# Optimization experiments

Measured on AMD Instinct MI355X. Metric: run time of the kernel, lower is better.

## Reference

```python
import jax, jax.numpy as jnp
import numpy as np

PAD_VAL = -999
N_TYPES = 8
D_IN, D_FF, D_FFC = 512, 1024, 512
B, S = 64, 512


def setup_inputs() -> dict:
    key = jax.random.key(0)
    ks = jax.random.split(key, 6)
    sc = 0.02
    return {
        "x": jax.random.normal(ks[0], (B, S, D_IN), dtype=jnp.float32),
        "sc_types": jax.random.randint(ks[1], (B, S), 0, N_TYPES, dtype=jnp.int64),
        "W_pre": jax.random.normal(ks[2], (D_IN, D_FF), dtype=jnp.float32) * sc,
        "W_types": jax.random.normal(ks[3], (N_TYPES, D_FF, D_IN), dtype=jnp.float32) * sc,
        "W_c1": jax.random.normal(ks[4], (D_IN, D_FFC), dtype=jnp.float32) * sc,
        "W_c2": jax.random.normal(ks[5], (D_FFC, 1), dtype=jnp.float32) * sc,
    }


def reference(x, sc_types, W_pre, W_types, W_c1, W_c2):
    # flatten tokens: [B*S, d_in], [B*S]
    x = x.reshape(-1, x.shape[-1])
    t = sc_types.reshape(-1)
    # (inputs contain no PAD_VAL tokens, so the pad mask is all-True and the
    # gather x[mask] is the identity; shapes stay static)
    x_ = jax.nn.relu(x @ W_pre)                       # [N, d_ff]
    # hard type routing: select per-type MLP output for each token
    x_types = jnp.zeros_like(x)
    for i in range(N_TYPES):
        yi = jax.nn.relu(x_ @ W_types[i])             # [N, d_in]
        x_types = jnp.where((t == i)[:, None], yi, x_types)
    x = x + x_types                                    # residual combine
    h = jax.nn.relu(x @ W_c1)                          # [N, d_ffc]
    return h @ W_c2                                    # [N, 1]
```

## Files before the change

kernel.cpp:

```cpp
#include <hip/hip_runtime.h>
#include <stdint.h>

#define N_TOK 32768
#define DIN   512
#define DFF   1024
#define MPAD  33792

__device__ __forceinline__ int rotk(int k, int row) {
    return (k & ~127) + (((k & 127) + ((row & 15) << 3)) & 127);
}

typedef __attribute__((ext_vector_type(8))) short bf16x8;
typedef __attribute__((ext_vector_type(4))) float f32x4;

__device__ __forceinline__ unsigned short f2bf(float f) {
    union { float f; unsigned int u; } v; v.f = f;
    unsigned int u = v.u;
    return (unsigned short)((u + 0x7FFFu + ((u >> 16) & 1u)) >> 16);
}
__device__ __forceinline__ float bf2f(unsigned int bits) {
    union { unsigned int u; float f; } v; v.u = bits << 16; return v.f;
}
__device__ __forceinline__ unsigned int pk4_fp8(float a, float b, float c, float d) {
    int v = __builtin_amdgcn_cvt_pk_fp8_f32(a, b, 0, false);
    v = __builtin_amdgcn_cvt_pk_fp8_f32(c, d, v, true);
    return (unsigned int)v;
}
__device__ __forceinline__ unsigned char f2fp8(float a) {
    return (unsigned char)(__builtin_amdgcn_cvt_pk_fp8_f32(a, a, 0, false) & 0xFF);
}

__device__ __forceinline__ void async16(const void* g, void* l) {
    __builtin_amdgcn_global_load_lds(
        (const __attribute__((address_space(1))) void*)g,
        (__attribute__((address_space(3))) void*)l, 16, 0, 0);
}

__global__ void prep_kernel(const float* __restrict__ x,
                            unsigned short* __restrict__ Xb,
                            unsigned char* __restrict__ Xb8,
                            const int* __restrict__ types,
                            int* __restrict__ blockhist,
                            const float* __restrict__ Wp,
                            const float* __restrict__ Wt,
                            const float* __restrict__ Wc,
                            unsigned char* __restrict__ Wp8,
                            unsigned char* __restrict__ Wt8,
                            unsigned short* __restrict__ WcT,
                            int* __restrict__ perm) {
    __shared__ float tile[32][33];
    __shared__ int lc[8];
    const int b = blockIdx.x, tid = threadIdx.x;
    if (b < 16384) {
        const int i = b * 1024 + tid * 4;
        float4 v = *(const float4*)(x + i);
        ushort4 o;
        o.x = f2bf(v.x); o.y = f2bf(v.y); o.z = f2bf(v.z); o.w = f2bf(v.w);
        *(ushort4*)(Xb + i) = o;
        const int row = i >> 9;
        const int k   = i & 511;
        *(unsigned int*)(Xb8 + (size_t)row * DIN + rotk(k, row)) = pk4_fp8(v.x, v.y, v.z, v.w);
        if (b < 64) {
            if (tid < 8) lc[tid] = 0;
            __syncthreads();
            atomicAdd(&lc[types[b * 512 + tid]], 1);
            atomicAdd(&lc[types[b * 512 + 256 + tid]], 1);
            __syncthreads();
            if (tid < 8) blockhist[b * 8 + tid] = lc[tid];
        }
    } else if (b < 26624) {
        const int r = b - 16384;
        const int z = r >> 10;
        const int bx = r & 31, by = (r >> 5) & 31;
        const int tx = tid & 31, ty = tid >> 5;
        const float* s; int K, N;
        if (z == 0)      { s = Wp;                          K = 512;  N = 1024; }
        else if (z <= 8) { s = Wt + (size_t)(z-1)*DIN*DFF;  K = 1024; N = 512; }
        else             { s = Wc;                          K = 512;  N = 512; }
        const int n0 = bx * 32, k0 = by * 32;
        if (n0 >= N || k0 >= K) return;
        for (int i = ty; i < 32; i += 8)
            tile[i][tx] = s[(size_t)(k0 + i) * N + n0 + tx];
        __syncthreads();
        if (z == 0) {
            for (int i = ty; i < 32; i += 8) {
                int n = n0 + i;
                Wp8[(size_t)n * K + rotk(k0 + tx, n)] = f2fp8(tile[tx][i] * 64.f);
            }
        } else if (z <= 8) {
            unsigned char* d = Wt8 + (size_t)(z-1)*DIN*DFF;
            for (int i = ty; i < 32; i += 8) {
                int n = n0 + i;
                d[(size_t)n * K + rotk(k0 + tx, n)] = f2fp8(tile[tx][i] * 64.f);
            }
        } else {
            for (int i = ty; i < 32; i += 8)
                WcT[(size_t)(n0 + i) * K + k0 + tx] = f2bf(tile[tx][i]);
        }
    } else {
        perm[(b - 26624) * 256 + tid] = -1;
    }
}

__global__ void scatter_kernel(const int* __restrict__ types,
                               const int* __restrict__ blockhist,
                               int* __restrict__ perm,
                               int* __restrict__ invperm,
                               float* __restrict__ outz,
                               int* __restrict__ po_out) {
    __shared__ int tots[8], base[8], fill[8];
    const int blk = blockIdx.x;
    const int tid = threadIdx.x;
    const int i = blk * 512 + tid;
    outz[i] = 0.f;
    int pre = 0;
    if (tid < 8) {
        int total = 0;
        for (int j = 0; j < 64; j++) {
            int v = blockhist[j * 8 + tid];
            if (j < blk) pre += v;
            total += v;
        }
        tots[tid] = total;
    }
    __syncthreads();
    if (tid < 8) {
        int off = 0, pob = 0;
        #pragma unroll
        for (int t2 = 0; t2 < 8; t2++) {
            if (t2 == tid) pob = off;
            off += ((tots[t2] + 127) >> 7) << 7;
        }
        base[tid] = pob + pre;
        fill[tid] = 0;
        if (blk == 0) {
            po_out[tid] = pob;
            if (tid == 0) po_out[8] = off;
        }
    }
    __syncthreads();
    const int t = types[i];
    const int r = atomicAdd(&fill[t], 1);
    const int p = base[t] + r;
    perm[p] = i;
    invperm[i] = p;
}

__global__ __launch_bounds__(512, 2)
void gemm1_fp8_8ph(const unsigned char* __restrict__ A,
                   const unsigned char* __restrict__ B,
                   unsigned char* __restrict__ C8,
                   const int* __restrict__ invperm) {
    __shared__ unsigned char As[2][256 * 128];
    __shared__ unsigned char Bs[2][256 * 128];
    __shared__ int ptile[256];

    const int tid  = threadIdx.x;
    const int wave = tid >> 6;
    const int lane = tid & 63;
    const int quad = lane >> 4;
    const int tl   = lane & 15;

    const int lin  = blockIdx.x;
    const int sid  = (lin & 7) * 64 + (lin >> 3);
    const int m0   = (sid >> 2) * 256;
    const int n0   = (sid & 3) * 256;

    const int wm = (wave & 1) * 128;
    const int wn = (wave >> 1) * 64;

    if (tid < 256) ptile[tid] = invperm[m0 + tid];

    f32x4 acc[8][4];
    #pragma unroll
    for (int i = 0; i < 8; i++)
        #pragma unroll
        for (int j = 0; j < 4; j++)
            acc[i][j] = (f32x4){0.f, 0.f, 0.f, 0.f};

    #pragma unroll
    for (int ci = 0; ci < 8; ++ci) {
        const int c = ci * 512 + tid;
        if (ci < 4) {
            const int row = c >> 3, j = c & 7;
            async16(A + (size_t)(m0 + row) * 512 + j * 16, &As[0][c * 16]);
        } else {
            const int c2 = c - 2048;
            const int row = c2 >> 3, j = c2 & 7;
            async16(B + (size_t)(n0 + row) * 512 + j * 16, &Bs[0][c2 * 16]);
        }
    }
    asm volatile("s_waitcnt vmcnt(0)" ::: "memory");
    __builtin_amdgcn_s_barrier();
    asm volatile("" ::: "memory");

    for (int t = 0; t < 4; ++t) {
        const unsigned char* Asl = As[t & 1];
        const unsigned char* Bsl = Bs[t & 1];
        unsigned char* Asn = As[(t + 1) & 1];
        unsigned char* Bsn = Bs[(t + 1) & 1];
        const int k0n = (t + 1) * 128;
        const bool st = (t < 3);
        #pragma unroll
        for (int ph = 0; ph < 8; ++ph) {
            const int ks = ph >> 1, mh = ph & 1;
            const int o = (ks * 32 + quad * 8 + tl * 8) & 127;
            long af[4], bfr[4];
            #pragma unroll
            for (int mt = 0; mt < 4; ++mt)
                af[mt] = *(const long*)(Asl + (wm + mh * 64 + mt * 16 + tl) * 128 + o);
            #pragma unroll
            for (int nt = 0; nt < 4; ++nt)
                bfr[nt] = *(const long*)(Bsl + (wn + nt * 16 + tl) * 128 + o);
            if (st && ph < 4) {
                #pragma unroll
                for (int u = 0; u < 2; ++u) {
                    const int cidx = ph * 2 + u;
                    const int c = cidx * 512 + tid;
                    if (cidx < 4) {
                        const int row = c >> 3, j = c & 7;
                        async16(A + (size_t)(m0 + row) * 512 + k0n + j * 16, Asn + c * 16);
                    } else {
                        const int c2 = c - 2048;
                        const int row = c2 >> 3, j = c2 & 7;
                        async16(B + (size_t)(n0 + row) * 512 + k0n + j * 16, Bsn + c2 * 16);
                    }
                }
            }
            __builtin_amdgcn_s_barrier();
            asm volatile("" ::: "memory");
            __builtin_amdgcn_s_setprio(1);
            #pragma unroll
            for (int mt = 0; mt < 4; ++mt)
                #pragma unroll
                for (int nt = 0; nt < 4; ++nt)
                    acc[mh * 4 + mt][nt] = __builtin_amdgcn_mfma_f32_16x16x32_fp8_fp8(
                        bfr[nt], af[mt], acc[mh * 4 + mt][nt], 0, 0, 0);
            __builtin_amdgcn_s_setprio(0);
            if (ph == 7) asm volatile("s_waitcnt vmcnt(0)" ::: "memory");
            __builtin_amdgcn_s_barrier();
            asm volatile("" ::: "memory");
        }
    }

    #pragma unroll
    for (int mh = 0; mh < 2; ++mh)
        #pragma unroll
        for (int mt = 0; mt < 4; ++mt) {
            const int p = ptile[wm + mh * 64 + mt * 16 + tl];
            const size_t rowbase = (size_t)p * DFF;
            const int prot = (p & 15) << 3;
            #pragma unroll
            for (int nt = 0; nt < 4; ++nt) {
                const int off = wn + nt * 16 + quad * 4;
                unsigned int pk = pk4_fp8(fmaxf(acc[mh * 4 + mt][nt][0], 0.f) * 0.125f,
                                          fmaxf(acc[mh * 4 + mt][nt][1], 0.f) * 0.125f,
                                          fmaxf(acc[mh * 4 + mt][nt][2], 0.f) * 0.125f,
                                          fmaxf(acc[mh * 4 + mt][nt][3], 0.f) * 0.125f);
                const int phys = (off & ~127) + (((off & 127) + prot) & 127);
                *(unsigned int*)(C8 + rowbase + n0 + phys) = pk;
            }
        }
}

template <int MODE>
__global__ __launch_bounds__(256, 4)
void gemm_fp8_kernel(const unsigned char* __restrict__ A,
                     const unsigned char* __restrict__ B,
                     void* __restrict__ Cout,
                     const unsigned short* __restrict__ xres,
                     const int* __restrict__ pmap,
                     const int* __restrict__ po,
                     int K, int ldA) {
    __shared__ unsigned char As[128 * 128];
    __shared__ unsigned char Bs[128 * 128];
    __shared__ int ptile[128];

    const int tid  = threadIdx.x;
    const int wave = tid >> 6;
    const int lane = tid & 63;
    const int quad = lane >> 4;
    const int tl   = lane & 15;
    const int m0 = blockIdx.y * 128;
    const int n0 = blockIdx.x * 128;
    const int wm = (wave & 1) * 64;
    const int wn = (wave >> 1) * 64;

    const unsigned char* Bp = B;
    if constexpr (MODE == 1) {
        if (m0 >= po[8]) return;
        int bsel = 0;
        #pragma unroll
        for (int i = 1; i < 8; i++) bsel += (m0 >= po[i]) ? 1 : 0;
        Bp = B + (size_t)bsel * (DIN * DFF);
    }
    if (tid < 128) ptile[tid] = pmap[m0 + tid];

    f32x4 acc[4][4];
    #pragma unroll
    for (int i = 0; i < 4; i++)
        #pragma unroll
        for (int j = 0; j < 4; j++)
            acc[i][j] = (f32x4){0.f, 0.f, 0.f, 0.f};

    for (int k0 = 0; k0 < K; k0 += 128) {
        __syncthreads();
        #pragma unroll
        for (int i = 0; i < 4; i++) {
            const int c   = (i * 4 + wave) * 64 + lane;
            const int row = c >> 3;
            const int j   = c & 7;
            async16(A + (size_t)(m0 + row) * ldA + k0 + j * 16, (char*)As + (size_t)c * 16);
        }
        #pragma unroll
        for (int i = 0; i < 4; i++) {
            const int c   = (i * 4 + wave) * 64 + lane;
            const int row = c >> 3;
            const int j   = c & 7;
            async16(Bp + (size_t)(n0 + row) * K + k0 + j * 16, (char*)Bs + (size_t)c * 16);
        }
        __syncthreads();

        #pragma unroll
        for (int ks = 0; ks < 4; ks++) {
            long af[4], bfr[4];
            const int o = (ks * 32 + quad * 8 + tl * 8) & 127;
            #pragma unroll
            for (int t = 0; t < 4; t++)
                af[t] = *(const long*)(As + (wm + t * 16 + tl) * 128 + o);
            #pragma unroll
            for (int t = 0; t < 4; t++)
                bfr[t] = *(const long*)(Bs + (wn + t * 16 + tl) * 128 + o);
            #pragma unroll
            for (int mt = 0; mt < 4; mt++)
                #pragma unroll
                for (int nt = 0; nt < 4; nt++)
                    acc[mt][nt] = __builtin_amdgcn_mfma_f32_16x16x32_fp8_fp8(
                        bfr[nt], af[mt], acc[mt][nt], 0, 0, 0);
        }
    }

    if constexpr (MODE == 0) {
        unsigned char* C8 = (unsigned char*)Cout;
        #pragma unroll
        for (int mt = 0; mt < 4; mt++) {
            const int p = ptile[wm + mt * 16 + tl];
            const size_t rowbase = (size_t)p * DFF;
            const int prot = (p & 15) << 3;
            #pragma unroll
            for (int nt = 0; nt < 4; nt++) {
                const int off = wn + nt * 16 + quad * 4;
                unsigned int pk = pk4_fp8(fmaxf(acc[mt][nt][0], 0.f) * 0.125f,
                                          fmaxf(acc[mt][nt][1], 0.f) * 0.125f,
                                          fmaxf(acc[mt][nt][2], 0.f) * 0.125f,
                                          fmaxf(acc[mt][nt][3], 0.f) * 0.125f);
                const int phys = (off & ~127) + (((off & 127) + prot) & 127);
                *(unsigned int*)(C8 + rowbase + n0 + phys) = pk;
            }
        }
    } else {
        unsigned short* Cb = (unsigned short*)Cout;
        #pragma unroll
        for (int mt = 0; mt < 4; mt++) {
            int tok = ptile[wm + mt * 16 + tl];
            if (tok < 0) continue;
            const size_t rowbase = (size_t)tok * DIN;
            #pragma unroll
            for (int nt = 0; nt < 4; nt++) {
                const int ncol = n0 + wn + nt * 16 + quad * 4;
                ushort4 rv = *(const ushort4*)(xres + rowbase + ncol);
                ushort4 o;
                o.x = f2bf(bf2f(rv.x) + fmaxf(acc[mt][nt][0], 0.f) * 0.001953125f);
                o.y = f2bf(bf2f(rv.y) + fmaxf(acc[mt][nt][1], 0.f) * 0.001953125f);
                o.z = f2bf(bf2f(rv.z) + fmaxf(acc[mt][nt][2], 0.f) * 0.001953125f);
                o.w = f2bf(bf2f(rv.w) + fmaxf(acc[mt][nt][3], 0.f) * 0.001953125f);
                *(ushort4*)(Cb + rowbase + ncol) = o;
            }
        }
    }
}

__global__ __launch_bounds__(512, 4)
void gemm3_kernel(const unsigned short* __restrict__ A,
                  const unsigned short* __restrict__ B,
                  const float* __restrict__ w2,
                  float* __restrict__ outp,
                  int K, int ldA) {
    __shared__ unsigned short As[128 * 64];
    __shared__ unsigned short Bs[256 * 64];

    const int tid  = threadIdx.x;
    const int wave = tid >> 6;
    const int lane = tid & 63;
    const int quad = lane >> 4;
    const int tl   = lane & 15;
    const int m0 = blockIdx.y * 128;
    const int n0 = blockIdx.x * 256;
    const int wm = (wave & 1) * 64;
    const int wn = (wave >> 1) * 64;

    f32x4 acc[4][4];
    #pragma unroll
    for (int i = 0; i < 4; i++)
        #pragma unroll
        for (int j = 0; j < 4; j++)
            acc[i][j] = (f32x4){0.f, 0.f, 0.f, 0.f};

    for (int k0 = 0; k0 < K; k0 += 64) {
        __syncthreads();
        #pragma unroll
        for (int i = 0; i < 2; i++) {
            const int c   = (i * 8 + wave) * 64 + lane;
            const int row = c >> 3;
            const int gj  = (c & 7) ^ (row & 7);
            async16(A + (size_t)(m0 + row) * ldA + k0 + gj * 8, (char*)As + (size_t)c * 16);
        }
        #pragma unroll
        for (int i = 0; i < 4; i++) {
            const int c   = (i * 8 + wave) * 64 + lane;
            const int row = c >> 3;
            const int gj  = (c & 7) ^ (row & 7);
            async16(B + (size_t)(n0 + row) * K + k0 + gj * 8, (char*)Bs + (size_t)c * 16);
        }
        __syncthreads();

        #pragma unroll
        for (int ks = 0; ks < 2; ks++) {
            bf16x8 af[4], bfr[4];
            const int jc = ks * 4 + quad;
            #pragma unroll
            for (int t = 0; t < 4; t++) {
                const int r = wm + t * 16 + tl;
                af[t] = *(const bf16x8*)(As + (r * 8 + (jc ^ (r & 7))) * 8);
            }
            #pragma unroll
            for (int t = 0; t < 4; t++) {
                const int r = wn + t * 16 + tl;
                bfr[t] = *(const bf16x8*)(Bs + (r * 8 + (jc ^ (r & 7))) * 8);
            }
            #pragma unroll
            for (int mt = 0; mt < 4; mt++)
                #pragma unroll
                for (int nt = 0; nt < 4; nt++)
                    acc[mt][nt] = __builtin_amdgcn_mfma_f32_16x16x32_bf16(
                        bfr[nt], af[mt], acc[mt][nt], 0, 0, 0);
        }
    }

    float4 w2v[4];
    #pragma unroll
    for (int nt = 0; nt < 4; nt++)
        w2v[nt] = *(const float4*)(w2 + n0 + wn + nt * 16 + quad * 4);
    #pragma unroll
    for (int mt = 0; mt < 4; mt++) {
        float s = 0.f;
        #pragma unroll
        for (int nt = 0; nt < 4; nt++) {
            s += fmaxf(acc[mt][nt][0], 0.f) * w2v[nt].x;
            s += fmaxf(acc[mt][nt][1], 0.f) * w2v[nt].y;
            s += fmaxf(acc[mt][nt][2], 0.f) * w2v[nt].z;
            s += fmaxf(acc[mt][nt][3], 0.f) * w2v[nt].w;
        }
        s += __shfl_down(s, 32);
        s += __shfl_down(s, 16);
        if (lane < 16) atomicAdd(&outp[m0 + wm + mt * 16 + lane], s);
    }
}

extern "C" void kernel_launch(void* const* d_in, const int* in_sizes, int n_in,
                              void* d_out, int out_size, void* d_ws, size_t ws_size,
                              hipStream_t stream) {
    const float* x      = (const float*)d_in[0];
    const int*   types  = (const int*)d_in[1];
    const float* W_pre  = (const float*)d_in[2];
    const float* W_types= (const float*)d_in[3];
    const float* W_c1   = (const float*)d_in[4];
    const float* W_c2   = (const float*)d_in[5];
    float* out = (float*)d_out;

    char* ws = (char*)d_ws;
    unsigned short* Xb  = (unsigned short*)(ws);
    unsigned char*  Xff8= (unsigned char*)(ws + 33554432ull);
    unsigned char*  Xb8 = (unsigned char*)(ws + 68157440ull);
    unsigned char*  Wp8 = (unsigned char*)(ws + 84934656ull);
    unsigned char*  Wt8 = (unsigned char*)(ws + 85458944ull);
    unsigned short* WcT = (unsigned short*)(ws + 89653248ull);
    int* perm           = (int*)(ws + 90177536ull);
    int* invperm        = (int*)(ws + 90312704ull);
    int* po             = (int*)(ws + 90443776ull);
    int* blockhist      = po + 16;

    prep_kernel<<<26756, 256, 0, stream>>>(x, Xb, Xb8, types, blockhist,
                                           W_pre, W_types, W_c1, Wp8, Wt8, WcT, perm);
    scatter_kernel<<<64, 512, 0, stream>>>(types, blockhist, perm, invperm, out, po);
    gemm1_fp8_8ph<<<512, 512, 0, stream>>>(Xb8, Wp8, Xff8, invperm);
    gemm_fp8_kernel<1><<<dim3(DIN / 128, MPAD / 128), 256, 0, stream>>>(
        Xff8, Wt8, Xb, Xb, perm, po, 1024, 1024);
    gemm3_kernel<<<dim3(DIN / 256, N_TOK / 128), 512, 0, stream>>>(
        Xb, WcT, W_c2, out, 512, 512);
}
```

Measured before the change: 232.8 us.

## Remap GEMM tile order for XCD locality, pack fp8 weight stores, batch residual loads

The grouped GEMM and the final GEMM move to 1D grids whose block index is remapped so that consecutive tiles sharing the same M rows land on the same XCD (blockIdx & 7 striping), aiming at better L2 reuse of A tiles. The weight prep for fp8 now packs four fp8 values into one 32-bit store per thread instead of byte stores. The residual epilogue issues all xres loads before the compute and store loop to expose memory-level parallelism. These changes hold more values in registers and rely on the XCD round-robin assumption.

Result: no change. 232.7 us (-0.0%).

```diff
diff --git a/kernel.cpp b/kernel.cpp
--- a/kernel.cpp
+++ b/kernel.cpp
@@ -82,17 +82,15 @@
         for (int i = ty; i < 32; i += 8)
             tile[i][tx] = s[(size_t)(k0 + i) * N + n0 + tx];
         __syncthreads();
-        if (z == 0) {
-            for (int i = ty; i < 32; i += 8) {
-                int n = n0 + i;
-                Wp8[(size_t)n * K + rotk(k0 + tx, n)] = f2fp8(tile[tx][i] * 64.f);
-            }
-        } else if (z <= 8) {
-            unsigned char* d = Wt8 + (size_t)(z-1)*DIN*DFF;
-            for (int i = ty; i < 32; i += 8) {
-                int n = n0 + i;
-                d[(size_t)n * K + rotk(k0 + tx, n)] = f2fp8(tile[tx][i] * 64.f);
-            }
+        if (z <= 8) {
+            unsigned char* d = (z == 0) ? Wp8 : (Wt8 + (size_t)(z-1)*DIN*DFF);
+            const int nl = tid >> 3;
+            const int k4 = (tid & 7) << 2;
+            const int n  = n0 + nl;
+            const int kk = k0 + k4;
+            unsigned int pk = pk4_fp8(tile[k4 + 0][nl] * 64.f, tile[k4 + 1][nl] * 64.f,
+                                      tile[k4 + 2][nl] * 64.f, tile[k4 + 3][nl] * 64.f);
+            *(unsigned int*)(d + (size_t)n * K + rotk(kk, n)) = pk;
         } else {
             for (int i = ty; i < 32; i += 8)
                 WcT[(size_t)(n0 + i) * K + k0 + tx] = f2bf(tile[tx][i]);
@@ -281,8 +279,15 @@
     const int lane = tid & 63;
     const int quad = lane >> 4;
     const int tl   = lane & 15;
-    const int m0 = blockIdx.y * 128;
-    const int n0 = blockIdx.x * 128;
+    int m0, n0;
+    if constexpr (MODE == 1) {
+        const int sid = (blockIdx.x & 7) * 132 + (blockIdx.x >> 3);
+        m0 = (sid >> 2) * 128;
+        n0 = (sid & 3) * 128;
+    } else {
+        m0 = blockIdx.y * 128;
+        n0 = blockIdx.x * 128;
+    }
     const int wm = (wave & 1) * 64;
     const int wn = (wave >> 1) * 64;
 
@@ -360,20 +365,30 @@
         }
     } else {
         unsigned short* Cb = (unsigned short*)Cout;
+        int toks[4];
+        #pragma unroll
+        for (int mt = 0; mt < 4; mt++) toks[mt] = ptile[wm + mt * 16 + tl];
+        ushort4 rv[4][4];
         #pragma unroll
         for (int mt = 0; mt < 4; mt++) {
-            int tok = ptile[wm + mt * 16 + tl];
-            if (tok < 0) continue;
-            const size_t rowbase = (size_t)tok * DIN;
+            if (toks[mt] < 0) continue;
+            const size_t rowbase = (size_t)toks[mt] * DIN;
+            #pragma unroll
+            for (int nt = 0; nt < 4; nt++)
+                rv[mt][nt] = *(const ushort4*)(xres + rowbase + n0 + wn + nt * 16 + quad * 4);
+        }
+        #pragma unroll
+        for (int mt = 0; mt < 4; mt++) {
+            if (toks[mt] < 0) continue;
+            const size_t rowbase = (size_t)toks[mt] * DIN;
             #pragma unroll
             for (int nt = 0; nt < 4; nt++) {
                 const int ncol = n0 + wn + nt * 16 + quad * 4;
-                ushort4 rv = *(const ushort4*)(xres + rowbase + ncol);
                 ushort4 o;
-                o.x = f2bf(bf2f(rv.x) + fmaxf(acc[mt][nt][0], 0.f) * 0.001953125f);
-                o.y = f2bf(bf2f(rv.y) + fmaxf(acc[mt][nt][1], 0.f) * 0.001953125f);
-                o.z = f2bf(bf2f(rv.z) + fmaxf(acc[mt][nt][2], 0.f) * 0.001953125f);
-                o.w = f2bf(bf2f(rv.w) + fmaxf(acc[mt][nt][3], 0.f) * 0.001953125f);
+                o.x = f2bf(bf2f(rv[mt][nt].x) + fmaxf(acc[mt][nt][0], 0.f) * 0.001953125f);
+                o.y = f2bf(bf2f(rv[mt][nt].y) + fmaxf(acc[mt][nt][1], 0.f) * 0.001953125f);
+                o.z = f2bf(bf2f(rv[mt][nt].z) + fmaxf(acc[mt][nt][2], 0.f) * 0.001953125f);
+                o.w = f2bf(bf2f(rv[mt][nt].w) + fmaxf(acc[mt][nt][3], 0.f) * 0.001953125f);
                 *(ushort4*)(Cb + rowbase + ncol) = o;
             }
         }
@@ -394,8 +409,9 @@
     const int lane = tid & 63;
     const int quad = lane >> 4;
     const int tl   = lane & 15;
-    const int m0 = blockIdx.y * 128;
-    const int n0 = blockIdx.x * 256;
+    const int sid = (blockIdx.x & 7) * 64 + (blockIdx.x >> 3);
+    const int m0 = (sid >> 1) * 128;
+    const int n0 = (sid & 1) * 256;
     const int wm = (wave & 1) * 64;
     const int wn = (wave >> 1) * 64;
 
@@ -494,8 +510,8 @@
                                            W_pre, W_types, W_c1, Wp8, Wt8, WcT, perm);
     scatter_kernel<<<64, 512, 0, stream>>>(types, blockhist, perm, invperm, out, po);
     gemm1_fp8_8ph<<<512, 512, 0, stream>>>(Xb8, Wp8, Xff8, invperm);
-    gemm_fp8_kernel<1><<<dim3(DIN / 128, MPAD / 128), 256, 0, stream>>>(
+    gemm_fp8_kernel<1><<<1056, 256, 0, stream>>>(
         Xff8, Wt8, Xb, Xb, perm, po, 1024, 1024);
-    gemm3_kernel<<<dim3(DIN / 256, N_TOK / 128), 512, 0, stream>>>(
+    gemm3_kernel<<<512, 512, 0, stream>>>(
         Xb, WcT, W_c2, out, 512, 512);
 }
```
